# Optimization experiments

Hardware: AMD Instinct MI355X
Metric: run time of the kernel (lower is better)

Reference implementation:

```python
import jax, jax.numpy as jnp
import numpy as np

B, T, D = 1, 4096, 2048
H, HKV = 16, 4
DH = D // H            # 128
GROUP = H // HKV       # 4
ROPE_BASE = 10000.0


def setup_inputs() -> dict:
    key = jax.random.key(0)
    kx, kq, kk, kv, ko = jax.random.split(key, 5)
    s = 0.02
    return {
        "x": jax.random.normal(kx, (B, T, D), dtype=jnp.float32),
        "Wq": jax.random.normal(kq, (D, D), dtype=jnp.float32) * s,
        "Wk": jax.random.normal(kk, (D, HKV * DH), dtype=jnp.float32) * s,
        "Wv": jax.random.normal(kv, (D, HKV * DH), dtype=jnp.float32) * s,
        "Wo": jax.random.normal(ko, (D, D), dtype=jnp.float32) * s,
    }


def _rope_sincos(t, half):
    inv_freq = 1.0 / (ROPE_BASE ** (jnp.arange(half, dtype=jnp.float32) / half))
    ang = jnp.arange(t, dtype=jnp.float32)[:, None] * inv_freq  # [T, half]
    # broadcast over batch and head dims: [1, T, 1, half]
    return jnp.sin(ang)[None, :, None, :], jnp.cos(ang)[None, :, None, :]


def _apply_rope(x, sin, cos, half):
    x1, x2 = x[..., :half], x[..., half:]
    return jnp.concatenate([x1 * cos - x2 * sin, x1 * sin + x2 * cos], axis=-1)


def reference(x, Wq, Wk, Wv, Wo):
    b, t, d = x.shape
    q = (x @ Wq).reshape(b, t, H, DH)      # [B,T,H,Dh], H ordered (Hkv, group)
    k = (x @ Wk).reshape(b, t, HKV, DH)    # [B,T,Hkv,Dh]
    v = (x @ Wv).reshape(b, t, HKV, DH)

    half = DH // 2
    sin, cos = _rope_sincos(t, half)
    q = _apply_rope(q, sin, cos, half)
    k = _apply_rope(k, sin, cos, half)

    # GQA without materializing repeated K/V: split q heads into (kv_head, group)
    qg = q.reshape(b, t, HKV, GROUP, DH)
    att = jnp.einsum('bthgd,bshd->bhgts', qg, k) / np.float32(np.sqrt(DH))
    causal = jnp.tril(jnp.ones((t, t), dtype=bool))
    att = jnp.where(causal[None, None, None, :, :], att, -jnp.inf)
    att = jax.nn.softmax(att, axis=-1)
    y = jnp.einsum('bhgts,bshd->bthgd', att, v).reshape(b, t, d)
    return y @ Wo
```

## Files before the change

### kernel.cpp

```cpp
#include <hip/hip_runtime.h>
#include <hip/hip_bf16.h>

#define TT 4096
#define DD 2048
#define NH 16
#define NKV 4
#define DHD 128
#define NQKV 3072

typedef __attribute__((ext_vector_type(8))) short short8;
typedef __attribute__((ext_vector_type(4))) float f32x4;
typedef __hip_bfloat16 bf16;

__global__ void cast_x_kernel(const float* __restrict__ x, bf16* __restrict__ xb, int n) {
    int i = (blockIdx.x * blockDim.x + threadIdx.x) * 4;
    if (i >= n) return;
    float4 v = *(const float4*)(x + i);
    xb[i + 0] = __float2bfloat16(v.x);
    xb[i + 1] = __float2bfloat16(v.y);
    xb[i + 2] = __float2bfloat16(v.z);
    xb[i + 3] = __float2bfloat16(v.w);
}

__global__ void transpose_cast_kernel(const float* __restrict__ in, bf16* __restrict__ out,
                                      int K, int N, int rowOff) {
    __shared__ float tile[32][33];
    int k0 = blockIdx.x * 32, n0 = blockIdx.y * 32;
    int tx = threadIdx.x, ty = threadIdx.y;
#pragma unroll
    for (int i = 0; i < 4; ++i)
        tile[ty + i * 8][tx] = in[(size_t)(k0 + ty + i * 8) * N + n0 + tx];
    __syncthreads();
#pragma unroll
    for (int i = 0; i < 4; ++i)
        out[(size_t)(rowOff + n0 + ty + i * 8) * K + k0 + tx] = __float2bfloat16(tile[tx][ty + i * 8]);
}

template <bool OUT_BF16>
__global__ __launch_bounds__(256) void gemm_bt_kernel(const bf16* __restrict__ A,
                                                      const bf16* __restrict__ Bt,
                                                      void* __restrict__ C,
                                                      int M, int N, int K) {
    __shared__ bf16 As[128][40];
    __shared__ bf16 Bs[128][40];
    int bn0 = blockIdx.x * 128, bm0 = blockIdx.y * 128;
    int tid = threadIdx.x;
    int wave = tid >> 6, lane = tid & 63, quad = lane >> 4, l15 = lane & 15;
    int wm = (wave >> 1) * 64, wn = (wave & 1) * 64;
    f32x4 zero = {0.f, 0.f, 0.f, 0.f};
    f32x4 acc[4][4];
#pragma unroll
    for (int i = 0; i < 4; ++i)
#pragma unroll
        for (int j = 0; j < 4; ++j) acc[i][j] = zero;

    for (int k0 = 0; k0 < K; k0 += 32) {
#pragma unroll
        for (int r = 0; r < 2; ++r) {
            int idx = r * 256 + tid;
            int row = idx >> 2, col = (idx & 3) * 8;
            *(short8*)&As[row][col] = *(const short8*)(A + (size_t)(bm0 + row) * K + k0 + col);
            *(short8*)&Bs[row][col] = *(const short8*)(Bt + (size_t)(bn0 + row) * K + k0 + col);
        }
        __syncthreads();
        short8 af[4], bfr[4];
#pragma unroll
        for (int i = 0; i < 4; ++i) af[i] = *(const short8*)&As[wm + i * 16 + l15][quad * 8];
#pragma unroll
        for (int j = 0; j < 4; ++j) bfr[j] = *(const short8*)&Bs[wn + j * 16 + l15][quad * 8];
#pragma unroll
        for (int i = 0; i < 4; ++i)
#pragma unroll
            for (int j = 0; j < 4; ++j)
                acc[i][j] = __builtin_amdgcn_mfma_f32_16x16x32_bf16(af[i], bfr[j], acc[i][j], 0, 0, 0);
        __syncthreads();
    }
#pragma unroll
    for (int i = 0; i < 4; ++i)
#pragma unroll
        for (int j = 0; j < 4; ++j)
#pragma unroll
            for (int r = 0; r < 4; ++r) {
                int row = bm0 + wm + i * 16 + quad * 4 + r;
                int col = bn0 + wn + j * 16 + l15;
                float v = acc[i][j][r];
                if (OUT_BF16)
                    ((bf16*)C)[(size_t)row * N + col] = __float2bfloat16(v);
                else
                    ((float*)C)[(size_t)row * N + col] = v;
            }
}

__global__ void rope_split_kernel(const bf16* __restrict__ QKV, bf16* __restrict__ Qs,
                                  bf16* __restrict__ Ks, bf16* __restrict__ Vt) {
    int slot = blockIdx.x * 4 + (threadIdx.x >> 6);
    int d = threadIdx.x & 63;
    int t = slot / 24, c = slot % 24;
    const bf16* base = QKV + (size_t)t * NQKV;
    int off = (c < 16) ? c * 128 : (c < 20) ? 2048 + (c - 16) * 128 : 2560 + (c - 20) * 128;
    float x1 = __bfloat162float(base[off + d]);
    float x2 = __bfloat162float(base[off + 64 + d]);
    float o1, o2;
    if (c < 20) {
        float invf = __expf((float)d * -0.14391156831f);
        float ang = (float)t * invf;
        float sn = sinf(ang), cs = cosf(ang);
        o1 = x1 * cs - x2 * sn;
        o2 = x1 * sn + x2 * cs;
    } else {
        o1 = x1;
        o2 = x2;
    }
    if (c < 16) {
        const float scale = 0.12751741f;
        o1 *= scale;
        o2 *= scale;
        bf16* dst = Qs + ((size_t)c * TT + t) * DHD;
        dst[d] = __float2bfloat16(o1);
        dst[d + 64] = __float2bfloat16(o2);
    } else if (c < 20) {
        bf16* dst = Ks + ((size_t)(c - 16) * TT + t) * DHD;
        dst[d] = __float2bfloat16(o1);
        dst[d + 64] = __float2bfloat16(o2);
    } else {
        int gg = c - 20;
        Vt[((size_t)gg * DHD + d) * TT + t] = __float2bfloat16(o1);
        Vt[((size_t)gg * DHD + d + 64) * TT + t] = __float2bfloat16(o2);
    }
}

__global__ __launch_bounds__(256, 3) void attn_kernel(const bf16* __restrict__ Qs,
                                                      const bf16* __restrict__ Ks,
                                                      const bf16* __restrict__ Vt,
                                                      bf16* __restrict__ Y) {
    __shared__ bf16 KsL[64][136];
    __shared__ bf16 VtL[128][72];
    __shared__ bf16 PsL[4][16][72];
    int h = blockIdx.y, bpair = blockIdx.x, g = h >> 2;
    int tid = threadIdx.x, wave = tid >> 6, lane = tid & 63, quad = lane >> 4, l15 = lane & 15;

    const bf16* kg = Ks + (size_t)g * TT * DHD;
    const bf16* vg = Vt + (size_t)g * DHD * TT;
    f32x4 zero = {0.f, 0.f, 0.f, 0.f};

    for (int pass = 0; pass < 2; ++pass) {
        int qt = (pass == 0) ? bpair : 63 - bpair;
        int qbase = qt * 64 + wave * 16;

        short8 qf[4];
        const bf16* qptr = Qs + ((size_t)h * TT + qbase + l15) * DHD + quad * 8;
#pragma unroll
        for (int ks = 0; ks < 4; ++ks) qf[ks] = *(const short8*)(qptr + ks * 32);

        f32x4 acc[8];
#pragma unroll
        for (int i = 0; i < 8; ++i) acc[i] = zero;
        float m_i[4] = {-1e30f, -1e30f, -1e30f, -1e30f};
        float l_i[4] = {0.f, 0.f, 0.f, 0.f};

        for (int kt = 0; kt <= qt; ++kt) {
            int kb = kt * 64;
            bool diag = (kt == qt);
            short8 kv[4], vv[4];
#pragma unroll
            for (int r = 0; r < 4; ++r) {
                int idx = r * 256 + tid;
                kv[r] = *(const short8*)(kg + (size_t)(kb + (idx >> 4)) * DHD + (idx & 15) * 8);
                vv[r] = *(const short8*)(vg + (size_t)(idx >> 3) * TT + kb + (idx & 7) * 8);
            }
            __syncthreads();
#pragma unroll
            for (int r = 0; r < 4; ++r) {
                int idx = r * 256 + tid;
                *(short8*)&KsL[idx >> 4][(idx & 15) * 8] = kv[r];
                *(short8*)&VtL[idx >> 3][(idx & 7) * 8] = vv[r];
            }
            __syncthreads();

            f32x4 s[4];
#pragma unroll
            for (int nt = 0; nt < 4; ++nt) {
                if (!diag || nt <= wave) {
                    s[nt] = zero;
#pragma unroll
                    for (int ks = 0; ks < 4; ++ks) {
                        short8 b = *(const short8*)&KsL[nt * 16 + l15][ks * 32 + quad * 8];
                        s[nt] = __builtin_amdgcn_mfma_f32_16x16x32_bf16(qf[ks], b, s[nt], 0, 0, 0);
                    }
                    if (diag && nt == wave) {
#pragma unroll
                        for (int r = 0; r < 4; ++r)
                            if (l15 > quad * 4 + r) s[nt][r] = -1e30f;
                    }
                } else {
#pragma unroll
                    for (int r = 0; r < 4; ++r) s[nt][r] = -1e30f;
                }
            }

            float alpha[4];
#pragma unroll
            for (int r = 0; r < 4; ++r) {
                float mt = fmaxf(fmaxf(s[0][r], s[1][r]), fmaxf(s[2][r], s[3][r]));
                mt = fmaxf(mt, __shfl_xor(mt, 1, 16));
                mt = fmaxf(mt, __shfl_xor(mt, 2, 16));
                mt = fmaxf(mt, __shfl_xor(mt, 4, 16));
                mt = fmaxf(mt, __shfl_xor(mt, 8, 16));
                float mnew = fmaxf(m_i[r], mt);
                alpha[r] = exp2f(m_i[r] - mnew);
                m_i[r] = mnew;
            }
#pragma unroll
            for (int nt = 0; nt < 4; ++nt)
#pragma unroll
                for (int r = 0; r < 4; ++r) s[nt][r] = exp2f(s[nt][r] - m_i[r]);
#pragma unroll
            for (int r = 0; r < 4; ++r) {
                float rs = (s[0][r] + s[1][r]) + (s[2][r] + s[3][r]);
                rs += __shfl_xor(rs, 1, 16);
                rs += __shfl_xor(rs, 2, 16);
                rs += __shfl_xor(rs, 4, 16);
                rs += __shfl_xor(rs, 8, 16);
                l_i[r] = l_i[r] * alpha[r] + rs;
            }
#pragma unroll
            for (int d8 = 0; d8 < 8; ++d8)
#pragma unroll
                for (int r = 0; r < 4; ++r) acc[d8][r] *= alpha[r];

#pragma unroll
            for (int nt = 0; nt < 4; ++nt)
#pragma unroll
                for (int r = 0; r < 4; ++r)
                    PsL[wave][quad * 4 + r][nt * 16 + l15] = __float2bfloat16(s[nt][r]);
            asm volatile("s_waitcnt lgkmcnt(0)" ::: "memory");

            int kkmax = diag ? (wave >> 1) + 1 : 2;
#pragma unroll
            for (int kk = 0; kk < 2; ++kk) {
                if (kk < kkmax) {
                    short8 pf = *(const short8*)&PsL[wave][l15][kk * 32 + quad * 8];
#pragma unroll
                    for (int d8 = 0; d8 < 8; ++d8) {
                        short8 b = *(const short8*)&VtL[d8 * 16 + l15][kk * 32 + quad * 8];
                        acc[d8] = __builtin_amdgcn_mfma_f32_16x16x32_bf16(pf, b, acc[d8], 0, 0, 0);
                    }
                }
            }
        }
#pragma unroll
        for (int r = 0; r < 4; ++r) l_i[r] = 1.0f / l_i[r];
#pragma unroll
        for (int d8 = 0; d8 < 8; ++d8)
#pragma unroll
            for (int r = 0; r < 4; ++r) {
                int t = qbase + quad * 4 + r;
                int dh = d8 * 16 + l15;
                Y[(size_t)t * DD + h * DHD + dh] = __float2bfloat16(acc[d8][r] * l_i[r]);
            }
        __syncthreads();
    }
}

extern "C" void kernel_launch(void* const* d_in, const int* in_sizes, int n_in,
                              void* d_out, int out_size, void* d_ws, size_t ws_size,
                              hipStream_t stream) {
    const float* x = (const float*)d_in[0];
    const float* Wq = (const float*)d_in[1];
    const float* Wk = (const float*)d_in[2];
    const float* Wv = (const float*)d_in[3];
    const float* Wo = (const float*)d_in[4];

    char* ws = (char*)d_ws;
    size_t off = 0;
    auto alloc = [&](size_t bytes) {
        void* p = ws + off;
        off += (bytes + 255) & ~(size_t)255;
        return p;
    };
    bf16* xb = (bf16*)alloc((size_t)TT * DD * 2);
    bf16* Wt = (bf16*)alloc((size_t)NQKV * DD * 2);
    bf16* Wot = (bf16*)alloc((size_t)DD * DD * 2);
    bf16* QKVb = (bf16*)alloc((size_t)TT * NQKV * 2);
    bf16* Qs = (bf16*)alloc((size_t)NH * TT * DHD * 2);
    bf16* Ksb = (bf16*)alloc((size_t)NKV * TT * DHD * 2);
    bf16* Vtb = (bf16*)alloc((size_t)NKV * DHD * TT * 2);
    bf16* Yb = (bf16*)alloc((size_t)TT * DD * 2);

    cast_x_kernel<<<(TT * DD / 4 + 255) / 256, 256, 0, stream>>>(x, xb, TT * DD);
    dim3 tb(32, 8);
    transpose_cast_kernel<<<dim3(DD / 32, DD / 32), tb, 0, stream>>>(Wq, Wt, DD, DD, 0);
    transpose_cast_kernel<<<dim3(DD / 32, 512 / 32), tb, 0, stream>>>(Wk, Wt, DD, 512, 2048);
    transpose_cast_kernel<<<dim3(DD / 32, 512 / 32), tb, 0, stream>>>(Wv, Wt, DD, 512, 2560);
    transpose_cast_kernel<<<dim3(DD / 32, DD / 32), tb, 0, stream>>>(Wo, Wot, DD, DD, 0);

    gemm_bt_kernel<true><<<dim3(NQKV / 128, TT / 128), 256, 0, stream>>>(xb, Wt, QKVb, TT, NQKV, DD);
    rope_split_kernel<<<TT * 24 / 4, 256, 0, stream>>>(QKVb, Qs, Ksb, Vtb);
    attn_kernel<<<dim3(32, NH), 256, 0, stream>>>(Qs, Ksb, Vtb, Yb);
    gemm_bt_kernel<false><<<dim3(DD / 128, TT / 128), 256, 0, stream>>>(Yb, Wot, d_out, TT, DD, DD);
}
```

Measured before the change: 460.0 us.

## Swizzle attention LDS, transpose MFMA operands, use direct global-to-LDS loads in GEMM

The attention kernel drops padded LDS arrays in favour of XOR-swizzled layouts and swaps the MFMA operand order, so each lane owns a single query row. This lets the softmax reductions use two cross-quad shuffles instead of four per row. Output is staged through LDS so Y is written with 16-byte stores, and the occupancy hint rises from 3 to 4. The GEMM now loads tiles with global_load_lds straight into unpadded LDS, which may add bank conflicts on the fragment reads, and the four weight transpose launches are merged into one kernel.

Result: faster. 420.5 us (-8.6%).

```diff
diff --git a/kernel.cpp b/kernel.cpp
--- a/kernel.cpp
+++ b/kernel.cpp
@@ -11,6 +11,11 @@
 typedef __attribute__((ext_vector_type(8))) short short8;
 typedef __attribute__((ext_vector_type(4))) float f32x4;
 typedef __hip_bfloat16 bf16;
+
+#define GLOAD_LDS16(g, l)                                                \
+    __builtin_amdgcn_global_load_lds(                                    \
+        (const __attribute__((address_space(1))) unsigned int*)(g),      \
+        (__attribute__((address_space(3))) unsigned int*)(l), 16, 0, 0)
 
 __global__ void cast_x_kernel(const float* __restrict__ x, bf16* __restrict__ xb, int n) {
     int i = (blockIdx.x * blockDim.x + threadIdx.x) * 4;
@@ -22,10 +27,22 @@
     xb[i + 3] = __float2bfloat16(v.w);
 }
 
-__global__ void transpose_cast_kernel(const float* __restrict__ in, bf16* __restrict__ out,
-                                      int K, int N, int rowOff) {
+__global__ void transpose_cast_all(const float* __restrict__ Wq, const float* __restrict__ Wk,
+                                   const float* __restrict__ Wv, const float* __restrict__ Wo,
+                                   bf16* __restrict__ Wt, bf16* __restrict__ Wot) {
     __shared__ float tile[32][33];
-    int k0 = blockIdx.x * 32, n0 = blockIdx.y * 32;
+    const float* in;
+    bf16* out;
+    int N, rowOff;
+    switch (blockIdx.z) {
+        case 0: in = Wq; out = Wt; N = 2048; rowOff = 0; break;
+        case 1: in = Wk; out = Wt; N = 512; rowOff = 2048; break;
+        case 2: in = Wv; out = Wt; N = 512; rowOff = 2560; break;
+        default: in = Wo; out = Wot; N = 2048; rowOff = 0; break;
+    }
+    int n0 = blockIdx.y * 32;
+    if (n0 >= N) return;
+    int k0 = blockIdx.x * 32;
     int tx = threadIdx.x, ty = threadIdx.y;
 #pragma unroll
     for (int i = 0; i < 4; ++i)
@@ -33,7 +50,7 @@
     __syncthreads();
 #pragma unroll
     for (int i = 0; i < 4; ++i)
-        out[(size_t)(rowOff + n0 + ty + i * 8) * K + k0 + tx] = __float2bfloat16(tile[tx][ty + i * 8]);
+        out[(size_t)(rowOff + n0 + ty + i * 8) * 2048 + k0 + tx] = __float2bfloat16(tile[tx][ty + i * 8]);
 }
 
 template <bool OUT_BF16>
@@ -41,12 +58,20 @@
                                                       const bf16* __restrict__ Bt,
                                                       void* __restrict__ C,
                                                       int M, int N, int K) {
-    __shared__ bf16 As[128][40];
-    __shared__ bf16 Bs[128][40];
+    __shared__ bf16 As[128 * 32];
+    __shared__ bf16 Bs[128 * 32];
     int bn0 = blockIdx.x * 128, bm0 = blockIdx.y * 128;
     int tid = threadIdx.x;
     int wave = tid >> 6, lane = tid & 63, quad = lane >> 4, l15 = lane & 15;
     int wm = (wave >> 1) * 64, wn = (wave & 1) * 64;
+
+    int srow = wave * 32 + (lane >> 2);
+    int scol = (lane & 3) * 8;
+    const bf16* gA = A + (size_t)(bm0 + srow) * K + scol;
+    const bf16* gB = Bt + (size_t)(bn0 + srow) * K + scol;
+    bf16* lA = As + srow * 32 + scol;
+    bf16* lB = Bs + srow * 32 + scol;
+
     f32x4 zero = {0.f, 0.f, 0.f, 0.f};
     f32x4 acc[4][4];
 #pragma unroll
@@ -55,19 +80,16 @@
         for (int j = 0; j < 4; ++j) acc[i][j] = zero;
 
     for (int k0 = 0; k0 < K; k0 += 32) {
-#pragma unroll
-        for (int r = 0; r < 2; ++r) {
-            int idx = r * 256 + tid;
-            int row = idx >> 2, col = (idx & 3) * 8;
-            *(short8*)&As[row][col] = *(const short8*)(A + (size_t)(bm0 + row) * K + k0 + col);
-            *(short8*)&Bs[row][col] = *(const short8*)(Bt + (size_t)(bn0 + row) * K + k0 + col);
-        }
+        GLOAD_LDS16(gA + k0, lA);
+        GLOAD_LDS16(gA + k0 + (size_t)16 * K, lA + 16 * 32);
+        GLOAD_LDS16(gB + k0, lB);
+        GLOAD_LDS16(gB + k0 + (size_t)16 * K, lB + 16 * 32);
         __syncthreads();
         short8 af[4], bfr[4];
 #pragma unroll
-        for (int i = 0; i < 4; ++i) af[i] = *(const short8*)&As[wm + i * 16 + l15][quad * 8];
-#pragma unroll
-        for (int j = 0; j < 4; ++j) bfr[j] = *(const short8*)&Bs[wn + j * 16 + l15][quad * 8];
+        for (int i = 0; i < 4; ++i) af[i] = *(const short8*)&As[(wm + i * 16 + l15) * 32 + quad * 8];
+#pragma unroll
+        for (int j = 0; j < 4; ++j) bfr[j] = *(const short8*)&Bs[(wn + j * 16 + l15) * 32 + quad * 8];
 #pragma unroll
         for (int i = 0; i < 4; ++i)
 #pragma unroll
@@ -129,13 +151,13 @@
     }
 }
 
-__global__ __launch_bounds__(256, 3) void attn_kernel(const bf16* __restrict__ Qs,
+__global__ __launch_bounds__(256, 4) void attn_kernel(const bf16* __restrict__ Qs,
                                                       const bf16* __restrict__ Ks,
                                                       const bf16* __restrict__ Vt,
                                                       bf16* __restrict__ Y) {
-    __shared__ bf16 KsL[64][136];
-    __shared__ bf16 VtL[128][72];
-    __shared__ bf16 PsL[4][16][72];
+    __shared__ bf16 KsL[64 * 128];
+    __shared__ bf16 VtL[128 * 64];
+    __shared__ bf16 PsL[4][16 * 64];
     int h = blockIdx.y, bpair = blockIdx.x, g = h >> 2;
     int tid = threadIdx.x, wave = tid >> 6, lane = tid & 63, quad = lane >> 4, l15 = lane & 15;
 
@@ -155,25 +177,28 @@
         f32x4 acc[8];
 #pragma unroll
         for (int i = 0; i < 8; ++i) acc[i] = zero;
-        float m_i[4] = {-1e30f, -1e30f, -1e30f, -1e30f};
-        float l_i[4] = {0.f, 0.f, 0.f, 0.f};
+        float m_i = -1e30f, l_i = 0.f;
 
         for (int kt = 0; kt <= qt; ++kt) {
             int kb = kt * 64;
             bool diag = (kt == qt);
             short8 kv[4], vv[4];
+            int krow[4], kc[4], vrow[4], vc[4];
 #pragma unroll
             for (int r = 0; r < 4; ++r) {
                 int idx = r * 256 + tid;
-                kv[r] = *(const short8*)(kg + (size_t)(kb + (idx >> 4)) * DHD + (idx & 15) * 8);
-                vv[r] = *(const short8*)(vg + (size_t)(idx >> 3) * TT + kb + (idx & 7) * 8);
+                krow[r] = idx >> 4;
+                kc[r] = idx & 15;
+                kv[r] = *(const short8*)(kg + (size_t)(kb + krow[r]) * DHD + kc[r] * 8);
+                vrow[r] = idx >> 3;
+                vc[r] = idx & 7;
+                vv[r] = *(const short8*)(vg + (size_t)vrow[r] * TT + kb + vc[r] * 8);
             }
             __syncthreads();
 #pragma unroll
             for (int r = 0; r < 4; ++r) {
-                int idx = r * 256 + tid;
-                *(short8*)&KsL[idx >> 4][(idx & 15) * 8] = kv[r];
-                *(short8*)&VtL[idx >> 3][(idx & 7) * 8] = vv[r];
+                *(short8*)&KsL[krow[r] * 128 + ((kc[r] ^ (krow[r] & 15)) * 8)] = kv[r];
+                *(short8*)&VtL[vrow[r] * 64 + ((vc[r] ^ (vrow[r] & 7)) * 8)] = vv[r];
             }
             __syncthreads();
 
@@ -184,13 +209,14 @@
                     s[nt] = zero;
 #pragma unroll
                     for (int ks = 0; ks < 4; ++ks) {
-                        short8 b = *(const short8*)&KsL[nt * 16 + l15][ks * 32 + quad * 8];
-                        s[nt] = __builtin_amdgcn_mfma_f32_16x16x32_bf16(qf[ks], b, s[nt], 0, 0, 0);
+                        int ch = (ks * 4 + quad) ^ l15;
+                        short8 kf = *(const short8*)&KsL[(nt * 16 + l15) * 128 + ch * 8];
+                        s[nt] = __builtin_amdgcn_mfma_f32_16x16x32_bf16(kf, qf[ks], s[nt], 0, 0, 0);
                     }
                     if (diag && nt == wave) {
 #pragma unroll
                         for (int r = 0; r < 4; ++r)
-                            if (l15 > quad * 4 + r) s[nt][r] = -1e30f;
+                            if (quad * 4 + r > l15) s[nt][r] = -1e30f;
                     }
                 } else {
 #pragma unroll
@@ -198,66 +224,82 @@
                 }
             }
 
-            float alpha[4];
-#pragma unroll
-            for (int r = 0; r < 4; ++r) {
-                float mt = fmaxf(fmaxf(s[0][r], s[1][r]), fmaxf(s[2][r], s[3][r]));
-                mt = fmaxf(mt, __shfl_xor(mt, 1, 16));
-                mt = fmaxf(mt, __shfl_xor(mt, 2, 16));
-                mt = fmaxf(mt, __shfl_xor(mt, 4, 16));
-                mt = fmaxf(mt, __shfl_xor(mt, 8, 16));
-                float mnew = fmaxf(m_i[r], mt);
-                alpha[r] = exp2f(m_i[r] - mnew);
-                m_i[r] = mnew;
-            }
+            float mloc = -1e30f;
 #pragma unroll
             for (int nt = 0; nt < 4; ++nt)
 #pragma unroll
-                for (int r = 0; r < 4; ++r) s[nt][r] = exp2f(s[nt][r] - m_i[r]);
-#pragma unroll
-            for (int r = 0; r < 4; ++r) {
-                float rs = (s[0][r] + s[1][r]) + (s[2][r] + s[3][r]);
-                rs += __shfl_xor(rs, 1, 16);
-                rs += __shfl_xor(rs, 2, 16);
-                rs += __shfl_xor(rs, 4, 16);
-                rs += __shfl_xor(rs, 8, 16);
-                l_i[r] = l_i[r] * alpha[r] + rs;
-            }
+                for (int r = 0; r < 4; ++r) mloc = fmaxf(mloc, s[nt][r]);
+            mloc = fmaxf(mloc, __shfl_xor(mloc, 16));
+            mloc = fmaxf(mloc, __shfl_xor(mloc, 32));
+            float mnew = fmaxf(m_i, mloc);
+            float alpha = exp2f(m_i - mnew);
+            m_i = mnew;
+            float sl = 0.f;
+#pragma unroll
+            for (int nt = 0; nt < 4; ++nt)
+#pragma unroll
+                for (int r = 0; r < 4; ++r) {
+                    s[nt][r] = exp2f(s[nt][r] - mnew);
+                    sl += s[nt][r];
+                }
+            sl += __shfl_xor(sl, 16);
+            sl += __shfl_xor(sl, 32);
+            l_i = l_i * alpha + sl;
 #pragma unroll
             for (int d8 = 0; d8 < 8; ++d8)
 #pragma unroll
-                for (int r = 0; r < 4; ++r) acc[d8][r] *= alpha[r];
+                for (int r = 0; r < 4; ++r) acc[d8][r] *= alpha;
 
 #pragma unroll
             for (int nt = 0; nt < 4; ++nt)
 #pragma unroll
-                for (int r = 0; r < 4; ++r)
-                    PsL[wave][quad * 4 + r][nt * 16 + l15] = __float2bfloat16(s[nt][r]);
+                for (int rr = 0; rr < 2; ++rr) {
+                    int col = nt * 16 + quad * 4 + rr * 2;
+                    int ch = (col >> 3) ^ (l15 & 7);
+                    __hip_bfloat162 pk;
+                    pk.x = __float2bfloat16(s[nt][rr * 2]);
+                    pk.y = __float2bfloat16(s[nt][rr * 2 + 1]);
+                    *(__hip_bfloat162*)&PsL[wave][l15 * 64 + ch * 8 + (col & 7)] = pk;
+                }
             asm volatile("s_waitcnt lgkmcnt(0)" ::: "memory");
 
             int kkmax = diag ? (wave >> 1) + 1 : 2;
 #pragma unroll
             for (int kk = 0; kk < 2; ++kk) {
                 if (kk < kkmax) {
-                    short8 pf = *(const short8*)&PsL[wave][l15][kk * 32 + quad * 8];
+                    int chp = (kk * 4 + quad) ^ (l15 & 7);
+                    short8 pf = *(const short8*)&PsL[wave][l15 * 64 + chp * 8];
 #pragma unroll
                     for (int d8 = 0; d8 < 8; ++d8) {
-                        short8 b = *(const short8*)&VtL[d8 * 16 + l15][kk * 32 + quad * 8];
-                        acc[d8] = __builtin_amdgcn_mfma_f32_16x16x32_bf16(pf, b, acc[d8], 0, 0, 0);
+                        short8 vf = *(const short8*)&VtL[(d8 * 16 + l15) * 64 + chp * 8];
+                        acc[d8] = __builtin_amdgcn_mfma_f32_16x16x32_bf16(vf, pf, acc[d8], 0, 0, 0);
                     }
                 }
             }
         }
-#pragma unroll
-        for (int r = 0; r < 4; ++r) l_i[r] = 1.0f / l_i[r];
+
+        float linv = 1.0f / l_i;
+        __syncthreads();
+        bf16* ow = KsL + wave * 2048;
 #pragma unroll
         for (int d8 = 0; d8 < 8; ++d8)
 #pragma unroll
-            for (int r = 0; r < 4; ++r) {
-                int t = qbase + quad * 4 + r;
-                int dh = d8 * 16 + l15;
-                Y[(size_t)t * DD + h * DHD + dh] = __float2bfloat16(acc[d8][r] * l_i[r]);
-            }
+            for (int rr = 0; rr < 2; ++rr) {
+                int colD = d8 * 16 + quad * 4 + rr * 2;
+                int ch = (colD >> 3) ^ (l15 & 7);
+                __hip_bfloat162 o2;
+                o2.x = __float2bfloat16(acc[d8][rr * 2] * linv);
+                o2.y = __float2bfloat16(acc[d8][rr * 2 + 1] * linv);
+                *(__hip_bfloat162*)&ow[l15 * 128 + ch * 8 + (colD & 7)] = o2;
+            }
+        asm volatile("s_waitcnt lgkmcnt(0)" ::: "memory");
+#pragma unroll
+        for (int c = 0; c < 4; ++c) {
+            int chunk = quad * 4 + c;
+            int ch = chunk ^ (l15 & 7);
+            short8 ov = *(const short8*)&ow[l15 * 128 + ch * 8];
+            *(short8*)&Y[(size_t)(qbase + l15) * DD + h * DHD + chunk * 8] = ov;
+        }
         __syncthreads();
     }
 }
@@ -288,11 +330,7 @@
     bf16* Yb = (bf16*)alloc((size_t)TT * DD * 2);
 
     cast_x_kernel<<<(TT * DD / 4 + 255) / 256, 256, 0, stream>>>(x, xb, TT * DD);
-    dim3 tb(32, 8);
-    transpose_cast_kernel<<<dim3(DD / 32, DD / 32), tb, 0, stream>>>(Wq, Wt, DD, DD, 0);
-    transpose_cast_kernel<<<dim3(DD / 32, 512 / 32), tb, 0, stream>>>(Wk, Wt, DD, 512, 2048);
-    transpose_cast_kernel<<<dim3(DD / 32, 512 / 32), tb, 0, stream>>>(Wv, Wt, DD, 512, 2560);
-    transpose_cast_kernel<<<dim3(DD / 32, DD / 32), tb, 0, stream>>>(Wo, Wot, DD, DD, 0);
+    transpose_cast_all<<<dim3(64, 64, 4), dim3(32, 8), 0, stream>>>(Wq, Wk, Wv, Wo, Wt, Wot);
 
     gemm_bt_kernel<true><<<dim3(NQKV / 128, TT / 128), 256, 0, stream>>>(xb, Wt, QKVb, TT, NQKV, DD);
     rope_split_kernel<<<TT * 24 / 4, 256, 0, stream>>>(QKVb, Qs, Ksb, Vtb);
```
